# Optimization experiments

Measured on AMD Instinct MI355X. Metric: run time of the kernel, lower is better.

The kernel has to match this reference:

```python
import jax, jax.numpy as jnp
import numpy as np

D_HEAD = 64  # per-head dim 'd' from init_kwargs


def layer_norm(x, g, b, eps=1e-5):
    m = x.mean(-1, keepdims=True)
    v = x.var(-1, keepdims=True)  # biased var, matches torch LayerNorm
    return (x - m) / jnp.sqrt(v + eps) * g + b


def setup_inputs() -> dict:
    key = jax.random.key(0)
    ks = jax.random.split(key, 16)
    F = 512
    B, T, N = 2, 8, 1024
    s = 1.0 / np.sqrt(F)
    u = lambda k, shape: jax.random.uniform(k, shape, jnp.float32, -s, s)
    return {
        "x": jax.random.normal(ks[0], (B, T, N, F), jnp.float32),
        "Wq": u(ks[1], (F, F)), "bq": u(ks[2], (F,)),
        "Wk": u(ks[3], (F, F)), "bk": u(ks[4], (F,)),
        "Wv": u(ks[5], (F, F)), "bv": u(ks[6], (F,)),
        "ln_g": jnp.ones((F,), jnp.float32), "ln_b": jnp.zeros((F,), jnp.float32),
        "W1": u(ks[7], (F, F)), "b1": u(ks[8], (F,)),
        "W2": u(ks[9], (F, F)), "b2": u(ks[10], (F,)),
        "lnff_g": jnp.ones((F,), jnp.float32), "lnff_b": jnp.zeros((F,), jnp.float32),
    }


def reference(x, Wq, bq, Wk, bk, Wv, bv, ln_g, ln_b, W1, b1, W2, b2, lnff_g, lnff_b):
    B, T, N, F = x.shape
    h = F // D_HEAD
    # q/k/v projections
    q = x @ Wq + bq
    k = x @ Wk + bk
    v = x @ Wv + bv
    # split last dim into heads (split+cat(dim=0) in torch == head axis here)
    qh = q.reshape(B, T, N, h, D_HEAD)
    kh = k.reshape(B, T, N, h, D_HEAD)
    vh = v.reshape(B, T, N, h, D_HEAD)
    # attention over node axis N per (batch, time, head)
    A = jnp.einsum('btqhd,btkhd->bthqk', qh, kh) / jnp.sqrt(jnp.asarray(D_HEAD, x.dtype))
    A = jax.nn.softmax(A, axis=-1)
    o = jnp.einsum('bthqk,btkhd->btqhd', A, vh).reshape(B, T, N, F)
    # residual + LN
    val = layer_norm(o + x, ln_g, ln_b)
    # FFN + final LN
    ff = jax.nn.relu(val @ W1 + b1) @ W2 + b2
    return layer_norm(ff, lnff_g, lnff_b)
```

## Files before the change

### kernel.cpp

```cpp
#include <hip/hip_runtime.h>
#include <hip/hip_bf16.h>

using bf16 = __hip_bfloat16;
typedef unsigned int u32x4 __attribute__((ext_vector_type(4)));
typedef float f32x4 __attribute__((ext_vector_type(4)));
typedef __bf16 bf16x8 __attribute__((ext_vector_type(8)));

#define DEVI __device__ __forceinline__

DEVI f32x4 mfma16(u32x4 a, u32x4 b, f32x4 c) {
    return __builtin_amdgcn_mfma_f32_16x16x32_bf16(
        __builtin_bit_cast(bf16x8, a), __builtin_bit_cast(bf16x8, b), c, 0, 0, 0);
}

struct bf8 { bf16 h[8]; };

DEVI u32x4 pack8(f32x4 lo, f32x4 hi) {
    bf8 t;
#pragma unroll
    for (int i = 0; i < 4; i++) {
        t.h[i] = __float2bfloat16(lo[i]);
        t.h[4 + i] = __float2bfloat16(hi[i]);
    }
    return __builtin_bit_cast(u32x4, t);
}

DEVI unsigned trunc2(float a, float b) {
    return __builtin_amdgcn_perm(__builtin_bit_cast(unsigned, b),
                                 __builtin_bit_cast(unsigned, a), 0x07060302);
}

DEVI void async16(const bf16* g, bf16* l) {
    __builtin_amdgcn_global_load_lds(
        (const __attribute__((address_space(1))) unsigned int*)g,
        (__attribute__((address_space(3))) unsigned int*)l, 16, 0, 0);
}

__global__ __launch_bounds__(256) void prep(
    const float* __restrict__ Wq, const float* __restrict__ Wk,
    const float* __restrict__ Wv, const float* __restrict__ W1,
    const float* __restrict__ W2, const float* __restrict__ x,
    bf16* __restrict__ WT, bf16* __restrict__ xb)
{
    int b = blockIdx.x;
    if (b < 5120) {
        int w = b >> 10;
        const float* src = (w == 0) ? Wq : (w == 1) ? Wk : (w == 2) ? Wv : (w == 3) ? W1 : W2;
        int idx = (b & 1023) * 256 + threadIdx.x;
        int n = idx >> 9, kk = idx & 511;
        WT[(size_t)w * 262144 + idx] = __float2bfloat16(src[kk * 512 + n]);
    } else {
        size_t i = ((size_t)(b - 5120) * 256 + threadIdx.x) * 8;
        f32x4 lo = *(const f32x4*)&x[i];
        f32x4 hi = *(const f32x4*)&x[i + 4];
        *(u32x4*)&xb[i] = pack8(lo, hi);
    }
}

__global__ __launch_bounds__(256) void gemm_qkv(
    const bf16* __restrict__ A, const bf16* __restrict__ WT,
    const float* __restrict__ bqp, const float* __restrict__ bkp, const float* __restrict__ bvp,
    bf16* __restrict__ qb, bf16* __restrict__ kb, bf16* __restrict__ vT)
{
    __shared__ __align__(16) bf16 As[128 * 32];
    __shared__ __align__(16) bf16 Bs[128 * 32];
    const int tid = threadIdx.x;
    const int lane = tid & 63, wave = tid >> 6;
    const int wm = (wave >> 1) * 64, wn = (wave & 1) * 64;
    const int wsel = blockIdx.y >> 2;
    const int bm = blockIdx.x * 128, bn = (blockIdx.y & 3) * 128;
    const bf16* Bt = WT + (size_t)wsel * 262144;
    const float* bias = (wsel == 0) ? bqp : (wsel == 1) ? bkp : bvp;
    const int lm = lane & 15, lq = lane >> 4;

    f32x4 acc[4][4];
#pragma unroll
    for (int i = 0; i < 4; i++)
#pragma unroll
        for (int j = 0; j < 4; j++) acc[i][j] = (f32x4){0.f, 0.f, 0.f, 0.f};

    for (int k0 = 0; k0 < 512; k0 += 32) {
        __syncthreads();
#pragma unroll
        for (int p = 0; p < 2; p++) {
            int c = p * 256 + tid;
            int r = c >> 2, kc = (c & 3) * 8;
            async16(&A[(size_t)(bm + r) * 512 + k0 + kc], &As[(p * 256 + wave * 64) * 8]);
            async16(&Bt[(size_t)(bn + r) * 512 + k0 + kc], &Bs[(p * 256 + wave * 64) * 8]);
        }
        __syncthreads();
        u32x4 af[4], bfr[4];
#pragma unroll
        for (int i = 0; i < 4; i++) af[i] = *(const u32x4*)&As[(wm + i * 16 + lm) * 32 + lq * 8];
#pragma unroll
        for (int j = 0; j < 4; j++) bfr[j] = *(const u32x4*)&Bs[(wn + j * 16 + lm) * 32 + lq * 8];
#pragma unroll
        for (int i = 0; i < 4; i++)
#pragma unroll
            for (int j = 0; j < 4; j++) acc[i][j] = mfma16(af[i], bfr[j], acc[i][j]);
    }

#pragma unroll
    for (int i = 0; i < 4; i++) {
#pragma unroll
        for (int j = 0; j < 4; j++) {
            int col = bn + wn + j * 16 + lm;
            float bv = bias[col];
#pragma unroll
            for (int r = 0; r < 4; r++) {
                int row = bm + wm + i * 16 + lq * 4 + r;
                float cv = acc[i][j][r] + bv;
                if (wsel == 0) {
                    qb[(size_t)row * 512 + col] = __float2bfloat16(cv * 0.18033688f);
                } else if (wsel == 1) {
                    kb[(size_t)row * 512 + col] = __float2bfloat16(cv);
                } else {
                    int bt = row >> 10, node = row & 1023;
                    int hh = col >> 6, d = col & 63;
                    vT[((size_t)((bt * 8 + hh) * 64 + d)) * 1024 + node] = __float2bfloat16(cv);
                }
            }
        }
    }
}

template <bool RELU>
__global__ __launch_bounds__(256) void gemm_bt(
    const bf16* __restrict__ A, const bf16* __restrict__ Bt,
    const float* __restrict__ bias, bf16* __restrict__ C)
{
    __shared__ __align__(16) bf16 As[128 * 32];
    __shared__ __align__(16) bf16 Bs[128 * 32];
    const int tid = threadIdx.x;
    const int lane = tid & 63, wave = tid >> 6;
    const int wm = (wave >> 1) * 64, wn = (wave & 1) * 64;
    const int bm = blockIdx.x * 128, bn = blockIdx.y * 128;
    const int lm = lane & 15, lq = lane >> 4;

    f32x4 acc[4][4];
#pragma unroll
    for (int i = 0; i < 4; i++)
#pragma unroll
        for (int j = 0; j < 4; j++) acc[i][j] = (f32x4){0.f, 0.f, 0.f, 0.f};

    for (int k0 = 0; k0 < 512; k0 += 32) {
        __syncthreads();
#pragma unroll
        for (int p = 0; p < 2; p++) {
            int c = p * 256 + tid;
            int r = c >> 2, kc = (c & 3) * 8;
            async16(&A[(size_t)(bm + r) * 512 + k0 + kc], &As[(p * 256 + wave * 64) * 8]);
            async16(&Bt[(size_t)(bn + r) * 512 + k0 + kc], &Bs[(p * 256 + wave * 64) * 8]);
        }
        __syncthreads();
        u32x4 af[4], bfr[4];
#pragma unroll
        for (int i = 0; i < 4; i++) af[i] = *(const u32x4*)&As[(wm + i * 16 + lm) * 32 + lq * 8];
#pragma unroll
        for (int j = 0; j < 4; j++) bfr[j] = *(const u32x4*)&Bs[(wn + j * 16 + lm) * 32 + lq * 8];
#pragma unroll
        for (int i = 0; i < 4; i++)
#pragma unroll
            for (int j = 0; j < 4; j++) acc[i][j] = mfma16(af[i], bfr[j], acc[i][j]);
    }

#pragma unroll
    for (int i = 0; i < 4; i++) {
#pragma unroll
        for (int j = 0; j < 4; j++) {
            int col = bn + wn + j * 16 + lm;
            float bv = bias[col];
#pragma unroll
            for (int r = 0; r < 4; r++) {
                int row = bm + wm + i * 16 + lq * 4 + r;
                float cv = acc[i][j][r] + bv;
                if (RELU) cv = fmaxf(cv, 0.f);
                C[(size_t)row * 512 + col] = __float2bfloat16(cv);
            }
        }
    }
}

__global__ __launch_bounds__(256) void attn_kernel(
    const bf16* __restrict__ q, const bf16* __restrict__ k,
    const bf16* __restrict__ vT, float* __restrict__ o)
{
    constexpr int KP = 72;
    constexpr int VP = 72;
    __shared__ __align__(16) bf16 Ks[64 * KP];
    __shared__ __align__(16) bf16 Vs[64 * VP];
    __shared__ __align__(16) bf16 Ps[4][64 * VP];

    const int tid = threadIdx.x, lane = tid & 63, wave = tid >> 6;
    const int group = blockIdx.x;
    const int bt = group >> 3, hh = group & 7;
    const int lm = lane & 15, lq = lane >> 4;
    const int qrow0 = bt * 1024 + blockIdx.y * 256 + wave * 64;

    u32x4 qf[4][2];
#pragma unroll
    for (int tm = 0; tm < 4; tm++)
#pragma unroll
        for (int kk2 = 0; kk2 < 2; kk2++)
            qf[tm][kk2] = *(const u32x4*)&q[(size_t)(qrow0 + tm * 16 + lm) * 512 + hh * 64 + kk2 * 32 + lq * 8];

    const bf16* kbase = k + (size_t)(bt * 1024) * 512 + hh * 64;
    const bf16* vbase = vT + (size_t)group * 64 * 1024;
    bf16* Pw = &Ps[wave][0];

    const int c0 = tid, c1 = 256 + tid;
    const int r0 = c0 >> 3, e0 = (c0 & 7) * 8;
    const int r1 = c1 >> 3, e1 = (c1 & 7) * 8;

    f32x4 accO[4][4];
#pragma unroll
    for (int tm = 0; tm < 4; tm++)
#pragma unroll
        for (int tn = 0; tn < 4; tn++) accO[tm][tn] = (f32x4){0.f, 0.f, 0.f, 0.f};
    float part[4] = {0.f, 0.f, 0.f, 0.f};

    u32x4 kreg0 = *(const u32x4*)&kbase[(size_t)r0 * 512 + e0];
    u32x4 kreg1 = *(const u32x4*)&kbase[(size_t)r1 * 512 + e1];
    u32x4 vreg0 = *(const u32x4*)&vbase[(size_t)r0 * 1024 + e0];
    u32x4 vreg1 = *(const u32x4*)&vbase[(size_t)r1 * 1024 + e1];

    for (int kt = 0; kt < 16; kt++) {
        __syncthreads();
        *(u32x4*)&Ks[r0 * KP + e0] = kreg0;
        *(u32x4*)&Ks[r1 * KP + e1] = kreg1;
        *(u32x4*)&Vs[r0 * VP + e0] = vreg0;
        *(u32x4*)&Vs[r1 * VP + e1] = vreg1;
        if (kt < 15) {
            const bf16* kn = kbase + (size_t)((kt + 1) * 64) * 512;
            const bf16* vn = vbase + (kt + 1) * 64;
            kreg0 = *(const u32x4*)&kn[(size_t)r0 * 512 + e0];
            kreg1 = *(const u32x4*)&kn[(size_t)r1 * 512 + e1];
            vreg0 = *(const u32x4*)&vn[(size_t)r0 * 1024 + e0];
            vreg1 = *(const u32x4*)&vn[(size_t)r1 * 1024 + e1];
        }
        __syncthreads();

#pragma unroll
        for (int tk = 0; tk < 4; tk++) {
            u32x4 kf0 = *(const u32x4*)&Ks[(tk * 16 + lm) * KP + lq * 8];
            u32x4 kf1 = *(const u32x4*)&Ks[(tk * 16 + lm) * KP + 32 + lq * 8];
#pragma unroll
            for (int tm = 0; tm < 4; tm++) {
                f32x4 st = (f32x4){0.f, 0.f, 0.f, 0.f};
                st = mfma16(kf0, qf[tm][0], st);
                st = mfma16(kf1, qf[tm][1], st);
                float p0 = __builtin_amdgcn_exp2f(st[0]);
                float p1 = __builtin_amdgcn_exp2f(st[1]);
                float p2 = __builtin_amdgcn_exp2f(st[2]);
                float p3 = __builtin_amdgcn_exp2f(st[3]);
                part[tm] += (p0 + p1) + (p2 + p3);
                unsigned lo = trunc2(p0, p1), hi = trunc2(p2, p3);
                unsigned long long pk2 = ((unsigned long long)hi << 32) | lo;
                *(unsigned long long*)&Pw[(tm * 16 + lm) * VP + tk * 16 + lq * 4] = pk2;
            }
        }

#pragma unroll
        for (int kc = 0; kc < 2; kc++) {
            u32x4 pf[4], vf[4];
#pragma unroll
            for (int tm = 0; tm < 4; tm++)
                pf[tm] = *(const u32x4*)&Pw[(tm * 16 + lm) * VP + kc * 32 + lq * 8];
#pragma unroll
            for (int tn = 0; tn < 4; tn++)
                vf[tn] = *(const u32x4*)&Vs[(tn * 16 + lm) * VP + kc * 32 + lq * 8];
#pragma unroll
            for (int tm = 0; tm < 4; tm++)
#pragma unroll
                for (int tn = 0; tn < 4; tn++)
                    accO[tm][tn] = mfma16(pf[tm], vf[tn], accO[tm][tn]);
        }
    }

#pragma unroll
    for (int tm = 0; tm < 4; tm++) {
        part[tm] += __shfl_xor(part[tm], 16);
        part[tm] += __shfl_xor(part[tm], 32);
    }
#pragma unroll
    for (int tm = 0; tm < 4; tm++)
#pragma unroll
        for (int r = 0; r < 4; r++) {
            float l = __shfl(part[tm], lq * 4 + r);
            float linv = 1.0f / l;
#pragma unroll
            for (int tn = 0; tn < 4; tn++) {
                int row = qrow0 + tm * 16 + lq * 4 + r;
                int col = hh * 64 + tn * 16 + lm;
                o[(size_t)row * 512 + col] = accO[tm][tn][r] * linv;
            }
        }
}

template <bool AF32, bool RES, bool OF32>
__global__ __launch_bounds__(256) void ln_kernel(
    const void* __restrict__ a, const float* __restrict__ res,
    const float* __restrict__ g, const float* __restrict__ bb, void* __restrict__ out)
{
    int row = blockIdx.x * 4 + (threadIdx.x >> 6);
    int lane = threadIdx.x & 63;
    size_t base = (size_t)row * 512 + lane * 8;
    int cbase = lane * 8;

    float x8[8];
    if (AF32) {
        const float* af = (const float*)a;
        f32x4 lo = *(const f32x4*)&af[base];
        f32x4 hi = *(const f32x4*)&af[base + 4];
#pragma unroll
        for (int i = 0; i < 4; i++) { x8[i] = lo[i]; x8[4 + i] = hi[i]; }
    } else {
        bf8 av = __builtin_bit_cast(bf8, *(const u32x4*)&((const bf16*)a)[base]);
#pragma unroll
        for (int i = 0; i < 8; i++) x8[i] = __bfloat162float(av.h[i]);
    }
    if (RES) {
        f32x4 lo = *(const f32x4*)&res[base];
        f32x4 hi = *(const f32x4*)&res[base + 4];
#pragma unroll
        for (int i = 0; i < 4; i++) { x8[i] += lo[i]; x8[4 + i] += hi[i]; }
    }

    float s = 0.f, s2 = 0.f;
#pragma unroll
    for (int i = 0; i < 8; i++) { s += x8[i]; s2 += x8[i] * x8[i]; }
#pragma unroll
    for (int off = 1; off < 64; off <<= 1) {
        s += __shfl_xor(s, off);
        s2 += __shfl_xor(s2, off);
    }
    float mean = s * (1.f / 512.f);
    float var = s2 * (1.f / 512.f) - mean * mean;
    float rstd = rsqrtf(var + 1e-5f);

    f32x4 g0 = *(const f32x4*)&g[cbase], g1 = *(const f32x4*)&g[cbase + 4];
    f32x4 b0 = *(const f32x4*)&bb[cbase], b1v = *(const f32x4*)&bb[cbase + 4];
    float y[8];
#pragma unroll
    for (int i = 0; i < 4; i++) {
        y[i] = (x8[i] - mean) * rstd * g0[i] + b0[i];
        y[4 + i] = (x8[4 + i] - mean) * rstd * g1[i] + b1v[i];
    }
    if (OF32) {
        float* op = (float*)out;
        *(f32x4*)&op[base] = (f32x4){y[0], y[1], y[2], y[3]};
        *(f32x4*)&op[base + 4] = (f32x4){y[4], y[5], y[6], y[7]};
    } else {
        bf8 ov;
#pragma unroll
        for (int i = 0; i < 8; i++) ov.h[i] = __float2bfloat16(y[i]);
        *(u32x4*)&((bf16*)out)[base] = __builtin_bit_cast(u32x4, ov);
    }
}

extern "C" void kernel_launch(void* const* d_in, const int* in_sizes, int n_in,
                              void* d_out, int out_size, void* d_ws, size_t ws_size,
                              hipStream_t stream)
{
    const float* x    = (const float*)d_in[0];
    const float* Wq   = (const float*)d_in[1];
    const float* bq   = (const float*)d_in[2];
    const float* Wk   = (const float*)d_in[3];
    const float* bk   = (const float*)d_in[4];
    const float* Wv   = (const float*)d_in[5];
    const float* bv   = (const float*)d_in[6];
    const float* ln_g = (const float*)d_in[7];
    const float* ln_b = (const float*)d_in[8];
    const float* W1   = (const float*)d_in[9];
    const float* b1   = (const float*)d_in[10];
    const float* W2   = (const float*)d_in[11];
    const float* b2   = (const float*)d_in[12];
    const float* lnffg = (const float*)d_in[13];
    const float* lnffb = (const float*)d_in[14];
    float* out = (float*)d_out;

    bf16* ws = (bf16*)d_ws;
    bf16* WT = ws;
    bf16* qb = ws + 5 * 262144;
    bf16* kb = qb + 8388608;
    bf16* vT = kb + 8388608;
    bf16* vl = qb;
    bf16* f1 = kb;
    bf16* f2 = vT;
    bf16* xb = (bf16*)d_out;

    prep<<<9216, 256, 0, stream>>>(Wq, Wk, Wv, W1, W2, x, WT, xb);

    gemm_qkv<<<dim3(128, 12), 256, 0, stream>>>(xb, WT, bq, bk, bv, qb, kb, vT);

    attn_kernel<<<dim3(128, 4), 256, 0, stream>>>(qb, kb, vT, out);

    ln_kernel<true, true, false><<<4096, 256, 0, stream>>>(out, x, ln_g, ln_b, vl);

    dim3 gg(128, 4);
    gemm_bt<true> <<<gg, 256, 0, stream>>>(vl, WT + 3 * 262144, b1, f1);
    gemm_bt<false><<<gg, 256, 0, stream>>>(f1, WT + 4 * 262144, b2, f2);

    ln_kernel<false, false, true><<<4096, 256, 0, stream>>>(f2, nullptr, lnffg, lnffb, out);
}
```

Measured before the change: 270.6 us.

## Register-prefetch GEMM tiles, vectorize epilogue stores, shrink attention blocks to two waves

The GEMM kernels stop using async global-to-LDS loads and instead prefetch the next K-slice into registers while the current tile is consumed. MFMA operands are swapped so each lane holds four consecutive columns, which allows packed 8-byte bf16 stores and vector bias loads in the epilogue. The V-transpose path now writes four contiguous nodes per store. The attention kernel drops from 4 to 2 waves per block and doubles the grid, with each thread staging more K/V rows, which adds register pressure in exchange for more blocks.

```diff
diff --git a/kernel.cpp b/kernel.cpp
--- a/kernel.cpp
+++ b/kernel.cpp
@@ -25,15 +25,16 @@
     return __builtin_bit_cast(u32x4, t);
 }
 
+DEVI unsigned long long pk4(float a, float b, float c, float d) {
+    union { unsigned long long u; bf16 h[4]; } t;
+    t.h[0] = __float2bfloat16(a); t.h[1] = __float2bfloat16(b);
+    t.h[2] = __float2bfloat16(c); t.h[3] = __float2bfloat16(d);
+    return t.u;
+}
+
 DEVI unsigned trunc2(float a, float b) {
     return __builtin_amdgcn_perm(__builtin_bit_cast(unsigned, b),
                                  __builtin_bit_cast(unsigned, a), 0x07060302);
-}
-
-DEVI void async16(const bf16* g, bf16* l) {
-    __builtin_amdgcn_global_load_lds(
-        (const __attribute__((address_space(1))) unsigned int*)g,
-        (__attribute__((address_space(3))) unsigned int*)l, 16, 0, 0);
 }
 
 __global__ __launch_bounds__(256) void prep(
@@ -73,52 +74,79 @@
     const float* bias = (wsel == 0) ? bqp : (wsel == 1) ? bkp : bvp;
     const int lm = lane & 15, lq = lane >> 4;
 
+    const int r0 = tid >> 2, kc0 = (tid & 3) * 8;
+    const bf16* Ap = A + (size_t)(bm + r0) * 512 + kc0;
+    const bf16* Bp = Bt + (size_t)(bn + r0) * 512 + kc0;
+
     f32x4 acc[4][4];
 #pragma unroll
     for (int i = 0; i < 4; i++)
 #pragma unroll
         for (int j = 0; j < 4; j++) acc[i][j] = (f32x4){0.f, 0.f, 0.f, 0.f};
 
+    u32x4 ar0 = *(const u32x4*)Ap;
+    u32x4 ar1 = *(const u32x4*)(Ap + 64 * 512);
+    u32x4 br0 = *(const u32x4*)Bp;
+    u32x4 br1 = *(const u32x4*)(Bp + 64 * 512);
+
     for (int k0 = 0; k0 < 512; k0 += 32) {
         __syncthreads();
-#pragma unroll
-        for (int p = 0; p < 2; p++) {
-            int c = p * 256 + tid;
-            int r = c >> 2, kc = (c & 3) * 8;
-            async16(&A[(size_t)(bm + r) * 512 + k0 + kc], &As[(p * 256 + wave * 64) * 8]);
-            async16(&Bt[(size_t)(bn + r) * 512 + k0 + kc], &Bs[(p * 256 + wave * 64) * 8]);
-        }
-        __syncthreads();
+        *(u32x4*)&As[r0 * 32 + kc0] = ar0;
+        *(u32x4*)&As[(r0 + 64) * 32 + kc0] = ar1;
+        *(u32x4*)&Bs[r0 * 32 + kc0] = br0;
+        *(u32x4*)&Bs[(r0 + 64) * 32 + kc0] = br1;
+        __syncthreads();
+        if (k0 < 480) {
+            ar0 = *(const u32x4*)(Ap + k0 + 32);
+            ar1 = *(const u32x4*)(Ap + 64 * 512 + k0 + 32);
+            br0 = *(const u32x4*)(Bp + k0 + 32);
+            br1 = *(const u32x4*)(Bp + 64 * 512 + k0 + 32);
+        }
         u32x4 af[4], bfr[4];
 #pragma unroll
         for (int i = 0; i < 4; i++) af[i] = *(const u32x4*)&As[(wm + i * 16 + lm) * 32 + lq * 8];
 #pragma unroll
         for (int j = 0; j < 4; j++) bfr[j] = *(const u32x4*)&Bs[(wn + j * 16 + lm) * 32 + lq * 8];
-#pragma unroll
-        for (int i = 0; i < 4; i++)
-#pragma unroll
-            for (int j = 0; j < 4; j++) acc[i][j] = mfma16(af[i], bfr[j], acc[i][j]);
-    }
-
-#pragma unroll
-    for (int i = 0; i < 4; i++) {
-#pragma unroll
-        for (int j = 0; j < 4; j++) {
-            int col = bn + wn + j * 16 + lm;
-            float bv = bias[col];
-#pragma unroll
-            for (int r = 0; r < 4; r++) {
-                int row = bm + wm + i * 16 + lq * 4 + r;
-                float cv = acc[i][j][r] + bv;
-                if (wsel == 0) {
-                    qb[(size_t)row * 512 + col] = __float2bfloat16(cv * 0.18033688f);
-                } else if (wsel == 1) {
-                    kb[(size_t)row * 512 + col] = __float2bfloat16(cv);
-                } else {
-                    int bt = row >> 10, node = row & 1023;
-                    int hh = col >> 6, d = col & 63;
-                    vT[((size_t)((bt * 8 + hh) * 64 + d)) * 1024 + node] = __float2bfloat16(cv);
-                }
+        if (wsel < 2) {
+#pragma unroll
+            for (int i = 0; i < 4; i++)
+#pragma unroll
+                for (int j = 0; j < 4; j++) acc[i][j] = mfma16(bfr[j], af[i], acc[i][j]);
+        } else {
+#pragma unroll
+            for (int i = 0; i < 4; i++)
+#pragma unroll
+                for (int j = 0; j < 4; j++) acc[i][j] = mfma16(af[i], bfr[j], acc[i][j]);
+        }
+    }
+
+    if (wsel < 2) {
+        const float scale = (wsel == 0) ? 0.18033688f : 1.0f;
+        bf16* dst = (wsel == 0) ? qb : kb;
+#pragma unroll
+        for (int i = 0; i < 4; i++) {
+#pragma unroll
+            for (int j = 0; j < 4; j++) {
+                int row = bm + wm + i * 16 + lm;
+                int colb = bn + wn + j * 16 + lq * 4;
+                f32x4 b4 = *(const f32x4*)&bias[colb];
+                *(unsigned long long*)&dst[(size_t)row * 512 + colb] =
+                    pk4((acc[i][j][0] + b4[0]) * scale, (acc[i][j][1] + b4[1]) * scale,
+                        (acc[i][j][2] + b4[2]) * scale, (acc[i][j][3] + b4[3]) * scale);
+            }
+        }
+    } else {
+#pragma unroll
+        for (int i = 0; i < 4; i++) {
+#pragma unroll
+            for (int j = 0; j < 4; j++) {
+                int col = bn + wn + j * 16 + lm;
+                float bv = bias[col];
+                int rowb = bm + wm + i * 16 + lq * 4;
+                int btq = rowb >> 10, node = rowb & 1023;
+                *(unsigned long long*)&vT[((size_t)((btq * 8 + (col >> 6)) * 64 + (col & 63))) * 1024 + node] =
+                    pk4(acc[i][j][0] + bv, acc[i][j][1] + bv,
+                        acc[i][j][2] + bv, acc[i][j][3] + bv);
             }
         }
     }
@@ -137,22 +165,34 @@
     const int bm = blockIdx.x * 128, bn = blockIdx.y * 128;
     const int lm = lane & 15, lq = lane >> 4;
 
+    const int r0 = tid >> 2, kc0 = (tid & 3) * 8;
+    const bf16* Ap = A + (size_t)(bm + r0) * 512 + kc0;
+    const bf16* Bp = Bt + (size_t)(bn + r0) * 512 + kc0;
+
     f32x4 acc[4][4];
 #pragma unroll
     for (int i = 0; i < 4; i++)
 #pragma unroll
         for (int j = 0; j < 4; j++) acc[i][j] = (f32x4){0.f, 0.f, 0.f, 0.f};
 
+    u32x4 ar0 = *(const u32x4*)Ap;
+    u32x4 ar1 = *(const u32x4*)(Ap + 64 * 512);
+    u32x4 br0 = *(const u32x4*)Bp;
+    u32x4 br1 = *(const u32x4*)(Bp + 64 * 512);
+
     for (int k0 = 0; k0 < 512; k0 += 32) {
         __syncthreads();
-#pragma unroll
-        for (int p = 0; p < 2; p++) {
-            int c = p * 256 + tid;
-            int r = c >> 2, kc = (c & 3) * 8;
-            async16(&A[(size_t)(bm + r) * 512 + k0 + kc], &As[(p * 256 + wave * 64) * 8]);
-            async16(&Bt[(size_t)(bn + r) * 512 + k0 + kc], &Bs[(p * 256 + wave * 64) * 8]);
-        }
-        __syncthreads();
+        *(u32x4*)&As[r0 * 32 + kc0] = ar0;
+        *(u32x4*)&As[(r0 + 64) * 32 + kc0] = ar1;
+        *(u32x4*)&Bs[r0 * 32 + kc0] = br0;
+        *(u32x4*)&Bs[(r0 + 64) * 32 + kc0] = br1;
+        __syncthreads();
+        if (k0 < 480) {
+            ar0 = *(const u32x4*)(Ap + k0 + 32);
+            ar1 = *(const u32x4*)(Ap + 64 * 512 + k0 + 32);
+            br0 = *(const u32x4*)(Bp + k0 + 32);
+            br1 = *(const u32x4*)(Bp + 64 * 512 + k0 + 32);
+        }
         u32x4 af[4], bfr[4];
 #pragma unroll
         for (int i = 0; i < 4; i++) af[i] = *(const u32x4*)&As[(wm + i * 16 + lm) * 32 + lq * 8];
@@ -161,27 +201,28 @@
 #pragma unroll
         for (int i = 0; i < 4; i++)
 #pragma unroll
-            for (int j = 0; j < 4; j++) acc[i][j] = mfma16(af[i], bfr[j], acc[i][j]);
+            for (int j = 0; j < 4; j++) acc[i][j] = mfma16(bfr[j], af[i], acc[i][j]);
     }
 
 #pragma unroll
     for (int i = 0; i < 4; i++) {
 #pragma unroll
         for (int j = 0; j < 4; j++) {
-            int col = bn + wn + j * 16 + lm;
-            float bv = bias[col];
-#pragma unroll
-            for (int r = 0; r < 4; r++) {
-                int row = bm + wm + i * 16 + lq * 4 + r;
-                float cv = acc[i][j][r] + bv;
-                if (RELU) cv = fmaxf(cv, 0.f);
-                C[(size_t)row * 512 + col] = __float2bfloat16(cv);
-            }
-        }
-    }
-}
-
-__global__ __launch_bounds__(256) void attn_kernel(
+            int row = bm + wm + i * 16 + lm;
+            int colb = bn + wn + j * 16 + lq * 4;
+            f32x4 b4 = *(const f32x4*)&bias[colb];
+            float c0 = acc[i][j][0] + b4[0], c1 = acc[i][j][1] + b4[1];
+            float c2 = acc[i][j][2] + b4[2], c3 = acc[i][j][3] + b4[3];
+            if (RELU) {
+                c0 = fmaxf(c0, 0.f); c1 = fmaxf(c1, 0.f);
+                c2 = fmaxf(c2, 0.f); c3 = fmaxf(c3, 0.f);
+            }
+            *(unsigned long long*)&C[(size_t)row * 512 + colb] = pk4(c0, c1, c2, c3);
+        }
+    }
+}
+
+__global__ __launch_bounds__(128, 2) void attn_kernel(
     const bf16* __restrict__ q, const bf16* __restrict__ k,
     const bf16* __restrict__ vT, float* __restrict__ o)
 {
@@ -189,13 +230,13 @@
     constexpr int VP = 72;
     __shared__ __align__(16) bf16 Ks[64 * KP];
     __shared__ __align__(16) bf16 Vs[64 * VP];
-    __shared__ __align__(16) bf16 Ps[4][64 * VP];
+    __shared__ __align__(16) bf16 Ps[2][64 * VP];
 
     const int tid = threadIdx.x, lane = tid & 63, wave = tid >> 6;
     const int group = blockIdx.x;
     const int bt = group >> 3, hh = group & 7;
     const int lm = lane & 15, lq = lane >> 4;
-    const int qrow0 = bt * 1024 + blockIdx.y * 256 + wave * 64;
+    const int qrow0 = bt * 1024 + blockIdx.y * 128 + wave * 64;
 
     u32x4 qf[4][2];
 #pragma unroll
@@ -206,11 +247,9 @@
 
     const bf16* kbase = k + (size_t)(bt * 1024) * 512 + hh * 64;
     const bf16* vbase = vT + (size_t)group * 64 * 1024;
-    bf16* Pw = &Ps[wave][0];
-
-    const int c0 = tid, c1 = 256 + tid;
-    const int r0 = c0 >> 3, e0 = (c0 & 7) * 8;
-    const int r1 = c1 >> 3, e1 = (c1 & 7) * 8;
+    bf16* Pw = Ps[wave];
+
+    const int rb = tid >> 3, e0 = (tid & 7) * 8;
 
     f32x4 accO[4][4];
 #pragma unroll
@@ -219,26 +258,30 @@
         for (int tn = 0; tn < 4; tn++) accO[tm][tn] = (f32x4){0.f, 0.f, 0.f, 0.f};
     float part[4] = {0.f, 0.f, 0.f, 0.f};
 
-    u32x4 kreg0 = *(const u32x4*)&kbase[(size_t)r0 * 512 + e0];
-    u32x4 kreg1 = *(const u32x4*)&kbase[(size_t)r1 * 512 + e1];
-    u32x4 vreg0 = *(const u32x4*)&vbase[(size_t)r0 * 1024 + e0];
-    u32x4 vreg1 = *(const u32x4*)&vbase[(size_t)r1 * 1024 + e1];
+    u32x4 kreg[4], vreg[4];
+#pragma unroll
+    for (int s = 0; s < 4; s++) {
+        kreg[s] = *(const u32x4*)&kbase[(size_t)(s * 16 + rb) * 512 + e0];
+        vreg[s] = *(const u32x4*)&vbase[(size_t)(s * 16 + rb) * 1024 + e0];
+    }
 
     for (int kt = 0; kt < 16; kt++) {
         __syncthreads();
-        *(u32x4*)&Ks[r0 * KP + e0] = kreg0;
-        *(u32x4*)&Ks[r1 * KP + e1] = kreg1;
-        *(u32x4*)&Vs[r0 * VP + e0] = vreg0;
-        *(u32x4*)&Vs[r1 * VP + e1] = vreg1;
+#pragma unroll
+        for (int s = 0; s < 4; s++) {
+            *(u32x4*)&Ks[(s * 16 + rb) * KP + e0] = kreg[s];
+            *(u32x4*)&Vs[(s * 16 + rb) * VP + e0] = vreg[s];
+        }
+        __syncthreads();
         if (kt < 15) {
             const bf16* kn = kbase + (size_t)((kt + 1) * 64) * 512;
             const bf16* vn = vbase + (kt + 1) * 64;
-            kreg0 = *(const u32x4*)&kn[(size_t)r0 * 512 + e0];
-            kreg1 = *(const u32x4*)&kn[(size_t)r1 * 512 + e1];
-            vreg0 = *(const u32x4*)&vn[(size_t)r0 * 1024 + e0];
-            vreg1 = *(const u32x4*)&vn[(size_t)r1 * 1024 + e1];
-        }
-        __syncthreads();
+#pragma unroll
+            for (int s = 0; s < 4; s++) {
+                kreg[s] = *(const u32x4*)&kn[(size_t)(s * 16 + rb) * 512 + e0];
+                vreg[s] = *(const u32x4*)&vn[(size_t)(s * 16 + rb) * 1024 + e0];
+            }
+        }
 
 #pragma unroll
         for (int tk = 0; tk < 4; tk++) {
@@ -393,7 +436,7 @@
 
     gemm_qkv<<<dim3(128, 12), 256, 0, stream>>>(xb, WT, bq, bk, bv, qb, kb, vT);
 
-    attn_kernel<<<dim3(128, 4), 256, 0, stream>>>(qb, kb, vT, out);
+    attn_kernel<<<dim3(128, 8), 128, 0, stream>>>(qb, kb, vT, out);
 
     ln_kernel<true, true, false><<<4096, 256, 0, stream>>>(out, x, ln_g, ln_b, vl);
 
```

Result: slower. 282.8 us (+4.5%).
